# Optimization experiments

Measured on AMD Instinct MI355X. Metric: run time of the kernel, lower is better.

## Reference

```python
import jax, jax.numpy as jnp
import numpy as np

N_NODES = 100000
N_EDGES = 3200000
IN_F, HID, OUT = 3, 32, 1
NEG_SLOPE = 0.2


def _glorot(key, shape):
    fan_in, fan_out = shape[0], shape[-1]
    lim = jnp.sqrt(6.0 / (fan_in + fan_out)).astype(jnp.float32)
    return jax.random.uniform(key, shape, jnp.float32, -lim, lim)


def setup_inputs() -> dict:
    key = jax.random.key(0)
    ks = jax.random.split(key, 12)
    x = jax.random.normal(ks[0], (N_NODES, IN_F), jnp.float32)
    edge_index = jax.random.randint(ks[1], (2, N_EDGES), 0, N_NODES, jnp.int32)
    return {
        "x": x,
        "edge_index": edge_index,
        "W1": _glorot(ks[2], (IN_F, HID)),
        "att_src1": _glorot(ks[3], (1, HID))[0],
        "att_dst1": _glorot(ks[4], (1, HID))[0],
        "b1": jnp.zeros((HID,), jnp.float32),
        "W2": _glorot(ks[5], (HID, HID)),
        "att_src2": _glorot(ks[6], (1, HID))[0],
        "att_dst2": _glorot(ks[7], (1, HID))[0],
        "b2": jnp.zeros((HID,), jnp.float32),
        "Wl": _glorot(ks[8], (HID, OUT)),
        "bl": jnp.zeros((OUT,), jnp.float32),
    }


def gat_layer(x, src, dst, W, att_src, att_dst, b):
    # h: [N, HID] dense transform
    h = x @ W
    # per-node attention halves (compute once per node, gather per edge)
    a_s = h @ att_src  # [N]
    a_d = h @ att_dst  # [N]
    logits = jax.nn.leaky_relu(a_s[src] + a_d[dst], NEG_SLOPE)  # [E+N]
    # segment-softmax over incoming edges of each dst node
    m = jax.ops.segment_max(logits, dst, num_segments=N_NODES)
    m = jnp.where(jnp.isfinite(m), m, 0.0)
    ex = jnp.exp(logits - m[dst])
    denom = jax.ops.segment_sum(ex, dst, num_segments=N_NODES)
    coef = ex / (denom[dst] + 1e-16)
    # weighted scatter-aggregate of source messages
    out = jax.ops.segment_sum(coef[:, None] * h[src], dst, num_segments=N_NODES)
    return out + b


def reference(x, edge_index, W1, att_src1, att_dst1, b1, W2, att_src2, att_dst2, b2, Wl, bl):
    # PyG GATConv default: add self-loops
    loops = jnp.arange(N_NODES, dtype=edge_index.dtype)
    src = jnp.concatenate([edge_index[0], loops])
    dst = jnp.concatenate([edge_index[1], loops])
    h = gat_layer(x, src, dst, W1, att_src1, att_dst1, b1)
    h = jax.nn.relu(h)  # dropout is identity in eval
    h = gat_layer(h, src, dst, W2, att_src2, att_dst2, b2)
    h = jax.nn.relu(h)
    return h @ Wl + bl
```

## Files before the change

kernel.cpp:

```cpp
#include <hip/hip_runtime.h>
#include <hip/hip_fp16.h>

#define HID 32
#define BN 131
#define NBPAD 768
#define BSTRIDE 4608
#define CHUNK 6144
#define EPT 12
#define CPAD 16
#define NSPLIT 3
#define HNMAX 44
#define LPCAP 1700

__device__ __forceinline__ float lrelu(float x) { return x > 0.0f ? x : 0.2f * x; }


__global__ void k_transform1(const float* __restrict__ x,
                             const float* __restrict__ W1,
                             const float* __restrict__ att_src,
                             const float* __restrict__ att_dst,
                             __half* __restrict__ hh,
                             float* __restrict__ a_s,
                             float* __restrict__ a_d,
                             int* __restrict__ cursor, int N)
{
    int tid = blockIdx.x * blockDim.x + threadIdx.x;
    if (tid < NBPAD * CPAD) cursor[tid] = 0;
    int n = tid >> 5, f = tid & 31;
    if (n >= N) return;
    float x0 = x[n * 3 + 0], x1 = x[n * 3 + 1], x2 = x[n * 3 + 2];
    float hv = x0 * W1[f] + x1 * W1[HID + f] + x2 * W1[2 * HID + f];
    hh[(size_t)n * HID + f] = __float2half(hv);
    float as = hv * att_src[f];
    float ad = hv * att_dst[f];
    #pragma unroll
    for (int m = 16; m >= 1; m >>= 1) {
        as += __shfl_xor(as, m, 32);
        ad += __shfl_xor(ad, m, 32);
    }
    if (f == 0) { a_s[n] = as; a_d[n] = ad; }
}


struct BinSM {
    int stage[CHUNK];
    unsigned short sbid[CHUNK];
    int lhist[NBPAD], lexcl[NBPAD], lbase[NBPAD], lcur[NBPAD];
    int arr[256];
};

__global__ void __launch_bounds__(512) k_binscatter(const int* __restrict__ src,
        const int* __restrict__ dst, int* __restrict__ cursor,
        unsigned int* __restrict__ packed, int NBr, int E)
{
    __shared__ BinSM S;
    int t = threadIdx.x;
    int base = blockIdx.x * CHUNK;
    int cnt = E - base; if (cnt > CHUNK) cnt = CHUNK;

    for (int i = t; i < NBPAD; i += 512) { S.lhist[i] = 0; S.lcur[i] = 0; }
    __syncthreads();

    int myd[EPT], mys[EPT];
    #pragma unroll
    for (int u = 0; u < EPT; ++u) {
        int i = t + u * 512;
        myd[u] = -1;
        if (i < cnt) { myd[u] = dst[base + i]; mys[u] = src[base + i]; }
    }
    #pragma unroll
    for (int u = 0; u < EPT; ++u)
        if (myd[u] >= 0) atomicAdd(&S.lhist[myd[u] / BN], 1);
    __syncthreads();

    int b0 = 3 * t;
    int c0 = 0, c1 = 0, c2 = 0, s = 0;
    if (t < 256) {
        c0 = S.lhist[b0]; c1 = S.lhist[b0 + 1]; c2 = S.lhist[b0 + 2];
        s = c0 + c1 + c2;
        S.arr[t] = s;
    }
    __syncthreads();
    for (int o = 1; o < 256; o <<= 1) {
        int v = (t < 256 && t >= o) ? S.arr[t - o] : 0;
        __syncthreads();
        if (t < 256) S.arr[t] += v;
        __syncthreads();
    }
    if (t < 256) {
        int ex = S.arr[t] - s;
        int e0 = ex, e1 = ex + c0, e2 = ex + c0 + c1;
        S.lexcl[b0] = e0; S.lexcl[b0 + 1] = e1; S.lexcl[b0 + 2] = e2;
        for (int i = 0; i < c0; ++i) S.sbid[e0 + i] = (unsigned short)b0;
        for (int i = 0; i < c1; ++i) S.sbid[e1 + i] = (unsigned short)(b0 + 1);
        for (int i = 0; i < c2; ++i) S.sbid[e2 + i] = (unsigned short)(b0 + 2);
    }
    for (int b = t; b < NBr; b += 512)
        if (S.lhist[b])
            S.lbase[b] = b * BSTRIDE + atomicAdd(&cursor[b * CPAD], S.lhist[b]);
    __syncthreads();

    #pragma unroll
    for (int u = 0; u < EPT; ++u) {
        if (myd[u] >= 0) {
            int d = myd[u];
            int b = d / BN;
            int dl = d - b * BN;
            int idx = S.lexcl[b] + atomicAdd(&S.lcur[b], 1);
            S.stage[idx] = (int)((unsigned)mys[u] | ((unsigned)dl << 17));
        }
    }
    __syncthreads();

    for (int i = t; i < cnt; i += 512) {
        int b = S.sbid[i];
        int gpos = S.lbase[b] + (i - S.lexcl[b]);
        if (gpos < (b + 1) * BSTRIDE)
            packed[gpos] = (unsigned)S.stage[i];
    }
}


struct AggSM {
    int2  lpair[LPCAP];
    int   hist[64], scn[64], cur[64];
    float adT[HNMAX];
};

__device__ __forceinline__ void build_slice(AggSM& S,
        const unsigned int* __restrict__ pk, int cnt,
        const float* __restrict__ a_s, const float* __restrict__ a_d,
        int nodeBase, int dlo, int HN, int N)
{
    int t = threadIdx.x;
    if (t < 64) { S.hist[t] = 0; S.cur[t] = 0; }
    if (t < HN) { int n = nodeBase + dlo + t; S.adT[t] = (n < N) ? a_d[n] : 0.0f; }
    __syncthreads();
    for (int i = t; i < cnt; i += 256) {
        unsigned ldl = ((pk[i] >> 17) & 255) - (unsigned)dlo;
        if (ldl < (unsigned)HN) atomicAdd(&S.hist[ldl], 1);
    }
    __syncthreads();
    if (t < 64) S.scn[t] = S.hist[t];
    __syncthreads();
    for (int o = 1; o < 64; o <<= 1) {
        int v = (t < 64 && t >= o) ? S.scn[t - o] : 0;
        __syncthreads();
        if (t < 64) S.scn[t] += v;
        __syncthreads();
    }
    for (int i = t; i < cnt; i += 256) {
        unsigned p = pk[i];
        unsigned ldl = ((p >> 17) & 255) - (unsigned)dlo;
        if (ldl < (unsigned)HN) {
            int sv = (int)(p & 0x1FFFF);
            float e = __expf(lrelu(a_s[sv] + S.adT[ldl]));
            int pos = atomicAdd(&S.cur[ldl], 1);
            int idx = (S.scn[ldl] - S.hist[ldl]) + pos;
            if (idx < LPCAP) S.lpair[idx] = make_int2(sv, __float_as_int(e));
        }
    }
    __syncthreads();
}

__device__ __forceinline__ void agg_node(const __half* __restrict__ hh,
                                         float ex_self, const float* __restrict__ b,
                                         int n, int f,
                                         const int2* lpair,
                                         int off, int dg, float& vx, float& vy)
{
    float den = ex_self;
    float2 hs = __half22float2(*(const __half2*)(hh + (size_t)n * HID + 2 * f));
    float accx = ex_self * hs.x;
    float accy = ex_self * hs.y;
    int j = 0;
    for (; j + 8 <= dg; j += 8) {
        int2 p0 = lpair[off + j + 0], p1 = lpair[off + j + 1];
        int2 p2 = lpair[off + j + 2], p3 = lpair[off + j + 3];
        int2 p4 = lpair[off + j + 4], p5 = lpair[off + j + 5];
        int2 p6 = lpair[off + j + 6], p7 = lpair[off + j + 7];
        __half2 h0 = *(const __half2*)(hh + (size_t)p0.x * HID + 2 * f);
        __half2 h1 = *(const __half2*)(hh + (size_t)p1.x * HID + 2 * f);
        __half2 h2 = *(const __half2*)(hh + (size_t)p2.x * HID + 2 * f);
        __half2 h3 = *(const __half2*)(hh + (size_t)p3.x * HID + 2 * f);
        __half2 h4 = *(const __half2*)(hh + (size_t)p4.x * HID + 2 * f);
        __half2 h5 = *(const __half2*)(hh + (size_t)p5.x * HID + 2 * f);
        __half2 h6 = *(const __half2*)(hh + (size_t)p6.x * HID + 2 * f);
        __half2 h7 = *(const __half2*)(hh + (size_t)p7.x * HID + 2 * f);
        float e0 = __int_as_float(p0.y), e1 = __int_as_float(p1.y);
        float e2 = __int_as_float(p2.y), e3 = __int_as_float(p3.y);
        float e4 = __int_as_float(p4.y), e5 = __int_as_float(p5.y);
        float e6 = __int_as_float(p6.y), e7 = __int_as_float(p7.y);
        float2 q0 = __half22float2(h0), q1 = __half22float2(h1);
        float2 q2 = __half22float2(h2), q3 = __half22float2(h3);
        float2 q4 = __half22float2(h4), q5 = __half22float2(h5);
        float2 q6 = __half22float2(h6), q7 = __half22float2(h7);
        den += ((e0 + e1) + (e2 + e3)) + ((e4 + e5) + (e6 + e7));
        accx = fmaf(e0, q0.x, accx); accy = fmaf(e0, q0.y, accy);
        accx = fmaf(e1, q1.x, accx); accy = fmaf(e1, q1.y, accy);
        accx = fmaf(e2, q2.x, accx); accy = fmaf(e2, q2.y, accy);
        accx = fmaf(e3, q3.x, accx); accy = fmaf(e3, q3.y, accy);
        accx = fmaf(e4, q4.x, accx); accy = fmaf(e4, q4.y, accy);
        accx = fmaf(e5, q5.x, accx); accy = fmaf(e5, q5.y, accy);
        accx = fmaf(e6, q6.x, accx); accy = fmaf(e6, q6.y, accy);
        accx = fmaf(e7, q7.x, accx); accy = fmaf(e7, q7.y, accy);
    }
    for (; j < dg; ++j) {
        int2 p0 = lpair[off + j];
        float e0 = __int_as_float(p0.y);
        float2 q0 = __half22float2(*(const __half2*)(hh + (size_t)p0.x * HID + 2 * f));
        den += e0;
        accx = fmaf(e0, q0.x, accx);
        accy = fmaf(e0, q0.y, accy);
    }
    float inv = 1.0f / (den + 1e-16f);
    vx = fmaxf(accx * inv + b[2 * f], 0.0f);
    vy = fmaxf(accy * inv + b[2 * f + 1], 0.0f);
}

__device__ __forceinline__ void epi_mid(int n, int f, float vx, float vy,
        const float* __restrict__ W2, const float* __restrict__ as2w,
        const float* __restrict__ ad2w,
        __half* __restrict__ hh_out, float* __restrict__ as_out,
        float* __restrict__ ad_out)
{
    float hx = 0.0f, hy = 0.0f;
    #pragma unroll
    for (int k = 0; k < 16; ++k) {
        float va = __shfl(vx, k, 16);
        float vb = __shfl(vy, k, 16);
        float2 w0 = *(const float2*)(W2 + (2 * k) * HID + 2 * f);
        float2 w1 = *(const float2*)(W2 + (2 * k + 1) * HID + 2 * f);
        hx = fmaf(va, w0.x, hx); hy = fmaf(va, w0.y, hy);
        hx = fmaf(vb, w1.x, hx); hy = fmaf(vb, w1.y, hy);
    }
    *(__half2*)(hh_out + (size_t)n * HID + 2 * f) = __floats2half2_rn(hx, hy);
    float as = hx * as2w[2 * f] + hy * as2w[2 * f + 1];
    float ad = hx * ad2w[2 * f] + hy * ad2w[2 * f + 1];
    #pragma unroll
    for (int m2 = 8; m2 >= 1; m2 >>= 1) {
        as += __shfl_xor(as, m2, 16);
        ad += __shfl_xor(ad, m2, 16);
    }
    if (f == 0) { as_out[n] = as; ad_out[n] = ad; }
}


__global__ void __launch_bounds__(256, 8) k_agg_mid(const __half* __restrict__ hh,
        const float* __restrict__ a_s, const float* __restrict__ a_d,
        const int* __restrict__ cursor, const unsigned int* __restrict__ packed,
        const float* __restrict__ b1, const float* __restrict__ W2,
        const float* __restrict__ as2w, const float* __restrict__ ad2w,
        __half* __restrict__ hh_out, float* __restrict__ as_out,
        float* __restrict__ ad_out, int N)
{
    __shared__ AggSM S;
    int bid = blockIdx.x, t = threadIdx.x;
    int bk = bid / NSPLIT, k = bid - NSPLIT * bk;
    int dlo = k * HNMAX;
    int HN = BN - dlo; if (HN > HNMAX) HN = HNMAX;
    int cnt = cursor[bk * CPAD]; if (cnt > BSTRIDE) cnt = BSTRIDE;
    build_slice(S, packed + (size_t)bk * BSTRIDE, cnt, a_s, a_d, bk * BN, dlo, HN, N);
    int g = t >> 4, f = t & 15;
    for (int ldl = g; ldl < HN; ldl += 16) {
        int n = bk * BN + dlo + ldl;
        if (n >= N) continue;
        int off = S.scn[ldl] - S.hist[ldl];
        int dg = S.hist[ldl];
        if (off + dg > LPCAP) dg = LPCAP - off;
        float exs = __expf(lrelu(a_s[n] + S.adT[ldl]));
        float vx, vy;
        agg_node(hh, exs, b1, n, f, S.lpair, off, dg, vx, vy);
        epi_mid(n, f, vx, vy, W2, as2w, ad2w, hh_out, as_out, ad_out);
    }
}

__global__ void __launch_bounds__(256, 8) k_agg_out(const __half* __restrict__ hh,
        const float* __restrict__ a_s, const float* __restrict__ a_d,
        const int* __restrict__ cursor, const unsigned int* __restrict__ packed,
        const float* __restrict__ b2, const float* __restrict__ Wl,
        const float* __restrict__ bl, float* __restrict__ out, int N)
{
    __shared__ AggSM S;
    int bid = blockIdx.x, t = threadIdx.x;
    int bk = bid / NSPLIT, k = bid - NSPLIT * bk;
    int dlo = k * HNMAX;
    int HN = BN - dlo; if (HN > HNMAX) HN = HNMAX;
    int cnt = cursor[bk * CPAD]; if (cnt > BSTRIDE) cnt = BSTRIDE;
    build_slice(S, packed + (size_t)bk * BSTRIDE, cnt, a_s, a_d, bk * BN, dlo, HN, N);
    int g = t >> 4, f = t & 15;
    for (int ldl = g; ldl < HN; ldl += 16) {
        int n = bk * BN + dlo + ldl;
        if (n >= N) continue;
        int off = S.scn[ldl] - S.hist[ldl];
        int dg = S.hist[ldl];
        if (off + dg > LPCAP) dg = LPCAP - off;
        float exs = __expf(lrelu(a_s[n] + S.adT[ldl]));
        float vx, vy;
        agg_node(hh, exs, b2, n, f, S.lpair, off, dg, vx, vy);
        float y = vx * Wl[2 * f] + vy * Wl[2 * f + 1];
        #pragma unroll
        for (int m2 = 8; m2 >= 1; m2 >>= 1)
            y += __shfl_xor(y, m2, 16);
        if (f == 0) out[n] = y + bl[0];
    }
}


extern "C" void kernel_launch(void* const* d_in, const int* in_sizes, int n_in,
                              void* d_out, int out_size, void* d_ws, size_t ws_size,
                              hipStream_t stream)
{
    const float* x        = (const float*)d_in[0];
    const int*   eidx     = (const int*)d_in[1];
    const float* W1       = (const float*)d_in[2];
    const float* att_src1 = (const float*)d_in[3];
    const float* att_dst1 = (const float*)d_in[4];
    const float* b1       = (const float*)d_in[5];
    const float* W2       = (const float*)d_in[6];
    const float* att_src2 = (const float*)d_in[7];
    const float* att_dst2 = (const float*)d_in[8];
    const float* b2       = (const float*)d_in[9];
    const float* Wl       = (const float*)d_in[10];
    const float* bl       = (const float*)d_in[11];
    float* out = (float*)d_out;

    int N = in_sizes[0] / 3;
    int E = in_sizes[1] / 2;
    const int* src = eidx;
    const int* dst = eidx + E;
    int NBr = (N + BN - 1) / BN;

    size_t szNHh = (size_t)N * HID * 2;
    size_t szN4  = (size_t)N * 4;
    size_t szPK  = (size_t)NBr * BSTRIDE * 4;

    char* ws = (char*)d_ws;
    __half* h1h    = (__half*)ws; ws += szNHh;
    __half* h2h    = (__half*)ws; ws += szNHh;
    unsigned int* packed = (unsigned int*)ws; ws += szPK;
    float*  a_s1   = (float*)ws;  ws += szN4;
    float*  a_d1   = (float*)ws;  ws += szN4;
    float*  a_s2   = (float*)ws;  ws += szN4;
    float*  a_d2   = (float*)ws;  ws += szN4;
    int*    cursor = (int*)ws;    ws += (size_t)NBPAD * CPAD * 4;

    const int B = 256;
    int gridNode32 = (N * HID + B - 1) / B;
    int gridBin    = (E + CHUNK - 1) / CHUNK;
    int gridAgg    = NBr * NSPLIT;

    k_transform1<<<gridNode32, B, 0, stream>>>(x, W1, att_src1, att_dst1,
                                               h1h, a_s1, a_d1, cursor, N);
    k_binscatter<<<gridBin, 512, 0, stream>>>(src, dst, cursor, packed, NBr, E);
    k_agg_mid<<<gridAgg, 256, 0, stream>>>(h1h, a_s1, a_d1, cursor, packed,
                                           b1, W2, att_src2, att_dst2,
                                           h2h, a_s2, a_d2, N);
    k_agg_out<<<gridAgg, 256, 0, stream>>>(h2h, a_s2, a_d2, cursor, packed,
                                           b2, Wl, bl, out, N);
}
```

Baseline: 288.3 us.

## Build full-bin CSR once per 512-thread block and software-pipeline neighbor gathers

Aggregation kernels stop splitting each destination bin across three blocks that each rescanned the whole packed bin. Now one 512-thread block builds the complete per-bin CSR in shared memory (36 KB pair buffer) and processes all 131 destinations. This removes the redundant bin scans and exp computations. The inner gather loop is also software-pipelined, loading the next 8 neighbors' features while accumulating the current 8. The trade-offs are larger shared memory, fewer blocks per CU, and more registers.

```diff
diff --git a/kernel.cpp b/kernel.cpp
--- a/kernel.cpp
+++ b/kernel.cpp
@@ -8,9 +8,6 @@
 #define CHUNK 6144
 #define EPT 12
 #define CPAD 16
-#define NSPLIT 3
-#define HNMAX 44
-#define LPCAP 1700
 
 __device__ __forceinline__ float lrelu(float x) { return x > 0.0f ? x : 0.2f * x; }
 
@@ -122,43 +119,38 @@
 
 
 struct AggSM {
-    int2  lpair[LPCAP];
-    int   hist[64], scn[64], cur[64];
-    float adT[HNMAX];
+    int2  lpair[BSTRIDE];
+    int   lhist[256], lscan[256], lcur[256];
+    float adT[BN];
 };
 
-__device__ __forceinline__ void build_slice(AggSM& S,
+__device__ __forceinline__ void build_csr(AggSM& S,
         const unsigned int* __restrict__ pk, int cnt,
         const float* __restrict__ a_s, const float* __restrict__ a_d,
-        int nodeBase, int dlo, int HN, int N)
+        int nodeBase, int N)
 {
     int t = threadIdx.x;
-    if (t < 64) { S.hist[t] = 0; S.cur[t] = 0; }
-    if (t < HN) { int n = nodeBase + dlo + t; S.adT[t] = (n < N) ? a_d[n] : 0.0f; }
-    __syncthreads();
-    for (int i = t; i < cnt; i += 256) {
-        unsigned ldl = ((pk[i] >> 17) & 255) - (unsigned)dlo;
-        if (ldl < (unsigned)HN) atomicAdd(&S.hist[ldl], 1);
-    }
-    __syncthreads();
-    if (t < 64) S.scn[t] = S.hist[t];
-    __syncthreads();
-    for (int o = 1; o < 64; o <<= 1) {
-        int v = (t < 64 && t >= o) ? S.scn[t - o] : 0;
+    if (t < 256) { S.lhist[t] = 0; S.lcur[t] = 0; }
+    if (t < BN) { int n = nodeBase + t; S.adT[t] = (n < N) ? a_d[n] : 0.0f; }
+    __syncthreads();
+    for (int i = t; i < cnt; i += 512)
+        atomicAdd(&S.lhist[(pk[i] >> 17) & 255], 1);
+    __syncthreads();
+    if (t < 256) S.lscan[t] = S.lhist[t];
+    __syncthreads();
+    for (int o = 1; o < 256; o <<= 1) {
+        int v = (t < 256 && t >= o) ? S.lscan[t - o] : 0;
         __syncthreads();
-        if (t < 64) S.scn[t] += v;
+        if (t < 256) S.lscan[t] += v;
         __syncthreads();
     }
-    for (int i = t; i < cnt; i += 256) {
+    for (int i = t; i < cnt; i += 512) {
         unsigned p = pk[i];
-        unsigned ldl = ((p >> 17) & 255) - (unsigned)dlo;
-        if (ldl < (unsigned)HN) {
-            int sv = (int)(p & 0x1FFFF);
-            float e = __expf(lrelu(a_s[sv] + S.adT[ldl]));
-            int pos = atomicAdd(&S.cur[ldl], 1);
-            int idx = (S.scn[ldl] - S.hist[ldl]) + pos;
-            if (idx < LPCAP) S.lpair[idx] = make_int2(sv, __float_as_int(e));
-        }
+        int dl = (p >> 17) & 255;
+        int sv = (int)(p & 0x1FFFF);
+        float e = __expf(lrelu(a_s[sv] + S.adT[dl]));
+        int pos = atomicAdd(&S.lcur[dl], 1);
+        S.lpair[(S.lscan[dl] - S.lhist[dl]) + pos] = make_int2(sv, __float_as_int(e));
     }
     __syncthreads();
 }
@@ -174,44 +166,87 @@
     float accx = ex_self * hs.x;
     float accy = ex_self * hs.y;
     int j = 0;
-    for (; j + 8 <= dg; j += 8) {
-        int2 p0 = lpair[off + j + 0], p1 = lpair[off + j + 1];
-        int2 p2 = lpair[off + j + 2], p3 = lpair[off + j + 3];
-        int2 p4 = lpair[off + j + 4], p5 = lpair[off + j + 5];
-        int2 p6 = lpair[off + j + 6], p7 = lpair[off + j + 7];
-        __half2 h0 = *(const __half2*)(hh + (size_t)p0.x * HID + 2 * f);
-        __half2 h1 = *(const __half2*)(hh + (size_t)p1.x * HID + 2 * f);
-        __half2 h2 = *(const __half2*)(hh + (size_t)p2.x * HID + 2 * f);
-        __half2 h3 = *(const __half2*)(hh + (size_t)p3.x * HID + 2 * f);
-        __half2 h4 = *(const __half2*)(hh + (size_t)p4.x * HID + 2 * f);
-        __half2 h5 = *(const __half2*)(hh + (size_t)p5.x * HID + 2 * f);
-        __half2 h6 = *(const __half2*)(hh + (size_t)p6.x * HID + 2 * f);
-        __half2 h7 = *(const __half2*)(hh + (size_t)p7.x * HID + 2 * f);
-        float e0 = __int_as_float(p0.y), e1 = __int_as_float(p1.y);
-        float e2 = __int_as_float(p2.y), e3 = __int_as_float(p3.y);
-        float e4 = __int_as_float(p4.y), e5 = __int_as_float(p5.y);
-        float e6 = __int_as_float(p6.y), e7 = __int_as_float(p7.y);
-        float2 q0 = __half22float2(h0), q1 = __half22float2(h1);
-        float2 q2 = __half22float2(h2), q3 = __half22float2(h3);
-        float2 q4 = __half22float2(h4), q5 = __half22float2(h5);
-        float2 q6 = __half22float2(h6), q7 = __half22float2(h7);
-        den += ((e0 + e1) + (e2 + e3)) + ((e4 + e5) + (e6 + e7));
-        accx = fmaf(e0, q0.x, accx); accy = fmaf(e0, q0.y, accy);
-        accx = fmaf(e1, q1.x, accx); accy = fmaf(e1, q1.y, accy);
-        accx = fmaf(e2, q2.x, accx); accy = fmaf(e2, q2.y, accy);
-        accx = fmaf(e3, q3.x, accx); accy = fmaf(e3, q3.y, accy);
-        accx = fmaf(e4, q4.x, accx); accy = fmaf(e4, q4.y, accy);
-        accx = fmaf(e5, q5.x, accx); accy = fmaf(e5, q5.y, accy);
-        accx = fmaf(e6, q6.x, accx); accy = fmaf(e6, q6.y, accy);
-        accx = fmaf(e7, q7.x, accx); accy = fmaf(e7, q7.y, accy);
+    if (dg >= 16) {
+        float e0, e1, e2, e3, e4, e5, e6, e7;
+        __half2 g0, g1, g2, g3, g4, g5, g6, g7;
+        {
+            int2 p0 = lpair[off + 0], p1 = lpair[off + 1];
+            int2 p2 = lpair[off + 2], p3 = lpair[off + 3];
+            int2 p4 = lpair[off + 4], p5 = lpair[off + 5];
+            int2 p6 = lpair[off + 6], p7 = lpair[off + 7];
+            g0 = *(const __half2*)(hh + (size_t)p0.x * HID + 2 * f);
+            g1 = *(const __half2*)(hh + (size_t)p1.x * HID + 2 * f);
+            g2 = *(const __half2*)(hh + (size_t)p2.x * HID + 2 * f);
+            g3 = *(const __half2*)(hh + (size_t)p3.x * HID + 2 * f);
+            g4 = *(const __half2*)(hh + (size_t)p4.x * HID + 2 * f);
+            g5 = *(const __half2*)(hh + (size_t)p5.x * HID + 2 * f);
+            g6 = *(const __half2*)(hh + (size_t)p6.x * HID + 2 * f);
+            g7 = *(const __half2*)(hh + (size_t)p7.x * HID + 2 * f);
+            e0 = __int_as_float(p0.y); e1 = __int_as_float(p1.y);
+            e2 = __int_as_float(p2.y); e3 = __int_as_float(p3.y);
+            e4 = __int_as_float(p4.y); e5 = __int_as_float(p5.y);
+            e6 = __int_as_float(p6.y); e7 = __int_as_float(p7.y);
+        }
+        for (; j + 16 <= dg; j += 8) {
+            int jb = off + j + 8;
+            int2 p0 = lpair[jb + 0], p1 = lpair[jb + 1];
+            int2 p2 = lpair[jb + 2], p3 = lpair[jb + 3];
+            int2 p4 = lpair[jb + 4], p5 = lpair[jb + 5];
+            int2 p6 = lpair[jb + 6], p7 = lpair[jb + 7];
+            __half2 t0 = *(const __half2*)(hh + (size_t)p0.x * HID + 2 * f);
+            __half2 t1 = *(const __half2*)(hh + (size_t)p1.x * HID + 2 * f);
+            __half2 t2 = *(const __half2*)(hh + (size_t)p2.x * HID + 2 * f);
+            __half2 t3 = *(const __half2*)(hh + (size_t)p3.x * HID + 2 * f);
+            __half2 t4 = *(const __half2*)(hh + (size_t)p4.x * HID + 2 * f);
+            __half2 t5 = *(const __half2*)(hh + (size_t)p5.x * HID + 2 * f);
+            __half2 t6 = *(const __half2*)(hh + (size_t)p6.x * HID + 2 * f);
+            __half2 t7 = *(const __half2*)(hh + (size_t)p7.x * HID + 2 * f);
+            float u0 = __int_as_float(p0.y), u1 = __int_as_float(p1.y);
+            float u2 = __int_as_float(p2.y), u3 = __int_as_float(p3.y);
+            float u4 = __int_as_float(p4.y), u5 = __int_as_float(p5.y);
+            float u6 = __int_as_float(p6.y), u7 = __int_as_float(p7.y);
+            float2 c0 = __half22float2(g0), c1 = __half22float2(g1);
+            float2 c2 = __half22float2(g2), c3 = __half22float2(g3);
+            float2 c4 = __half22float2(g4), c5 = __half22float2(g5);
+            float2 c6 = __half22float2(g6), c7 = __half22float2(g7);
+            den += ((e0 + e1) + (e2 + e3)) + ((e4 + e5) + (e6 + e7));
+            accx = fmaf(e0, c0.x, accx); accy = fmaf(e0, c0.y, accy);
+            accx = fmaf(e1, c1.x, accx); accy = fmaf(e1, c1.y, accy);
+            accx = fmaf(e2, c2.x, accx); accy = fmaf(e2, c2.y, accy);
+            accx = fmaf(e3, c3.x, accx); accy = fmaf(e3, c3.y, accy);
+            accx = fmaf(e4, c4.x, accx); accy = fmaf(e4, c4.y, accy);
+            accx = fmaf(e5, c5.x, accx); accy = fmaf(e5, c5.y, accy);
+            accx = fmaf(e6, c6.x, accx); accy = fmaf(e6, c6.y, accy);
+            accx = fmaf(e7, c7.x, accx); accy = fmaf(e7, c7.y, accy);
+            e0 = u0; e1 = u1; e2 = u2; e3 = u3;
+            e4 = u4; e5 = u5; e6 = u6; e7 = u7;
+            g0 = t0; g1 = t1; g2 = t2; g3 = t3;
+            g4 = t4; g5 = t5; g6 = t6; g7 = t7;
+        }
+        {
+            float2 c0 = __half22float2(g0), c1 = __half22float2(g1);
+            float2 c2 = __half22float2(g2), c3 = __half22float2(g3);
+            float2 c4 = __half22float2(g4), c5 = __half22float2(g5);
+            float2 c6 = __half22float2(g6), c7 = __half22float2(g7);
+            den += ((e0 + e1) + (e2 + e3)) + ((e4 + e5) + (e6 + e7));
+            accx = fmaf(e0, c0.x, accx); accy = fmaf(e0, c0.y, accy);
+            accx = fmaf(e1, c1.x, accx); accy = fmaf(e1, c1.y, accy);
+            accx = fmaf(e2, c2.x, accx); accy = fmaf(e2, c2.y, accy);
+            accx = fmaf(e3, c3.x, accx); accy = fmaf(e3, c3.y, accy);
+            accx = fmaf(e4, c4.x, accx); accy = fmaf(e4, c4.y, accy);
+            accx = fmaf(e5, c5.x, accx); accy = fmaf(e5, c5.y, accy);
+            accx = fmaf(e6, c6.x, accx); accy = fmaf(e6, c6.y, accy);
+            accx = fmaf(e7, c7.x, accx); accy = fmaf(e7, c7.y, accy);
+        }
+        j += 8;
     }
     for (; j < dg; ++j) {
         int2 p0 = lpair[off + j];
-        float e0 = __int_as_float(p0.y);
-        float2 q0 = __half22float2(*(const __half2*)(hh + (size_t)p0.x * HID + 2 * f));
-        den += e0;
-        accx = fmaf(e0, q0.x, accx);
-        accy = fmaf(e0, q0.y, accy);
+        float ee = __int_as_float(p0.y);
+        float2 cc = __half22float2(*(const __half2*)(hh + (size_t)p0.x * HID + 2 * f));
+        den += ee;
+        accx = fmaf(ee, cc.x, accx);
+        accy = fmaf(ee, cc.y, accy);
     }
     float inv = 1.0f / (den + 1e-16f);
     vx = fmaxf(accx * inv + b[2 * f], 0.0f);
@@ -246,7 +281,7 @@
 }
 
 
-__global__ void __launch_bounds__(256, 8) k_agg_mid(const __half* __restrict__ hh,
+__global__ void __launch_bounds__(512) k_agg_mid(const __half* __restrict__ hh,
         const float* __restrict__ a_s, const float* __restrict__ a_d,
         const int* __restrict__ cursor, const unsigned int* __restrict__ packed,
         const float* __restrict__ b1, const float* __restrict__ W2,
@@ -255,47 +290,39 @@
         float* __restrict__ ad_out, int N)
 {
     __shared__ AggSM S;
-    int bid = blockIdx.x, t = threadIdx.x;
-    int bk = bid / NSPLIT, k = bid - NSPLIT * bk;
-    int dlo = k * HNMAX;
-    int HN = BN - dlo; if (HN > HNMAX) HN = HNMAX;
+    int bk = blockIdx.x, t = threadIdx.x;
     int cnt = cursor[bk * CPAD]; if (cnt > BSTRIDE) cnt = BSTRIDE;
-    build_slice(S, packed + (size_t)bk * BSTRIDE, cnt, a_s, a_d, bk * BN, dlo, HN, N);
+    build_csr(S, packed + (size_t)bk * BSTRIDE, cnt, a_s, a_d, bk * BN, N);
     int g = t >> 4, f = t & 15;
-    for (int ldl = g; ldl < HN; ldl += 16) {
-        int n = bk * BN + dlo + ldl;
+    for (int dl = g; dl < BN; dl += 32) {
+        int n = bk * BN + dl;
         if (n >= N) continue;
-        int off = S.scn[ldl] - S.hist[ldl];
-        int dg = S.hist[ldl];
-        if (off + dg > LPCAP) dg = LPCAP - off;
-        float exs = __expf(lrelu(a_s[n] + S.adT[ldl]));
+        int off = S.lscan[dl] - S.lhist[dl];
+        int dg = S.lhist[dl];
+        float exs = __expf(lrelu(a_s[n] + S.adT[dl]));
         float vx, vy;
         agg_node(hh, exs, b1, n, f, S.lpair, off, dg, vx, vy);
         epi_mid(n, f, vx, vy, W2, as2w, ad2w, hh_out, as_out, ad_out);
     }
 }
 
-__global__ void __launch_bounds__(256, 8) k_agg_out(const __half* __restrict__ hh,
+__global__ void __launch_bounds__(512) k_agg_out(const __half* __restrict__ hh,
         const float* __restrict__ a_s, const float* __restrict__ a_d,
         const int* __restrict__ cursor, const unsigned int* __restrict__ packed,
         const float* __restrict__ b2, const float* __restrict__ Wl,
         const float* __restrict__ bl, float* __restrict__ out, int N)
 {
     __shared__ AggSM S;
-    int bid = blockIdx.x, t = threadIdx.x;
-    int bk = bid / NSPLIT, k = bid - NSPLIT * bk;
-    int dlo = k * HNMAX;
-    int HN = BN - dlo; if (HN > HNMAX) HN = HNMAX;
+    int bk = blockIdx.x, t = threadIdx.x;
     int cnt = cursor[bk * CPAD]; if (cnt > BSTRIDE) cnt = BSTRIDE;
-    build_slice(S, packed + (size_t)bk * BSTRIDE, cnt, a_s, a_d, bk * BN, dlo, HN, N);
+    build_csr(S, packed + (size_t)bk * BSTRIDE, cnt, a_s, a_d, bk * BN, N);
     int g = t >> 4, f = t & 15;
-    for (int ldl = g; ldl < HN; ldl += 16) {
-        int n = bk * BN + dlo + ldl;
+    for (int dl = g; dl < BN; dl += 32) {
+        int n = bk * BN + dl;
         if (n >= N) continue;
-        int off = S.scn[ldl] - S.hist[ldl];
-        int dg = S.hist[ldl];
-        if (off + dg > LPCAP) dg = LPCAP - off;
-        float exs = __expf(lrelu(a_s[n] + S.adT[ldl]));
+        int off = S.lscan[dl] - S.lhist[dl];
+        int dg = S.lhist[dl];
+        float exs = __expf(lrelu(a_s[n] + S.adT[dl]));
         float vx, vy;
         agg_node(hh, exs, b2, n, f, S.lpair, off, dg, vx, vy);
         float y = vx * Wl[2 * f] + vy * Wl[2 * f + 1];
@@ -348,14 +375,13 @@
     const int B = 256;
     int gridNode32 = (N * HID + B - 1) / B;
     int gridBin    = (E + CHUNK - 1) / CHUNK;
-    int gridAgg    = NBr * NSPLIT;
 
     k_transform1<<<gridNode32, B, 0, stream>>>(x, W1, att_src1, att_dst1,
                                                h1h, a_s1, a_d1, cursor, N);
     k_binscatter<<<gridBin, 512, 0, stream>>>(src, dst, cursor, packed, NBr, E);
-    k_agg_mid<<<gridAgg, 256, 0, stream>>>(h1h, a_s1, a_d1, cursor, packed,
-                                           b1, W2, att_src2, att_dst2,
-                                           h2h, a_s2, a_d2, N);
-    k_agg_out<<<gridAgg, 256, 0, stream>>>(h2h, a_s2, a_d2, cursor, packed,
-                                           b2, Wl, bl, out, N);
-}
+    k_agg_mid<<<NBr, 512, 0, stream>>>(h1h, a_s1, a_d1, cursor, packed,
+                                       b1, W2, att_src2, att_dst2,
+                                       h2h, a_s2, a_d2, N);
+    k_agg_out<<<NBr, 512, 0, stream>>>(h2h, a_s2, a_d2, cursor, packed,
+                                       b2, Wl, bl, out, N);
+}
```

Result: faster. 248.6 us (-13.8%).

## Replace 3-way bin slicing with one 512-thread block per smaller bin

Applied to the files above, without the earlier changes.

Each aggregation block used to rescan a whole 131-node bin's packed edges three times, once per 44-node slice. Now bins hold 98 nodes, and one 512-thread block builds the full per-bin CSR once and aggregates all nodes. This removes redundant packed-edge reads and filtering. In exchange it uses more shared memory per block (lpair of 3584 int2), runs a larger scan, and launches fewer, bigger blocks, which may lower occupancy.

```diff
diff --git a/kernel.cpp b/kernel.cpp
--- a/kernel.cpp
+++ b/kernel.cpp
@@ -2,15 +2,12 @@
 #include <hip/hip_fp16.h>
 
 #define HID 32
-#define BN 131
-#define NBPAD 768
-#define BSTRIDE 4608
+#define BN 98
+#define NBPAD 1024
+#define BSTRIDE 3584
 #define CHUNK 6144
 #define EPT 12
 #define CPAD 16
-#define NSPLIT 3
-#define HNMAX 44
-#define LPCAP 1700
 
 __device__ __forceinline__ float lrelu(float x) { return x > 0.0f ? x : 0.2f * x; }
 
@@ -73,11 +70,12 @@
         if (myd[u] >= 0) atomicAdd(&S.lhist[myd[u] / BN], 1);
     __syncthreads();
 
-    int b0 = 3 * t;
-    int c0 = 0, c1 = 0, c2 = 0, s = 0;
+    int b0 = 4 * t;
+    int c0 = 0, c1 = 0, c2 = 0, c3 = 0, s = 0;
     if (t < 256) {
-        c0 = S.lhist[b0]; c1 = S.lhist[b0 + 1]; c2 = S.lhist[b0 + 2];
-        s = c0 + c1 + c2;
+        c0 = S.lhist[b0]; c1 = S.lhist[b0 + 1];
+        c2 = S.lhist[b0 + 2]; c3 = S.lhist[b0 + 3];
+        s = c0 + c1 + c2 + c3;
         S.arr[t] = s;
     }
     __syncthreads();
@@ -89,11 +87,13 @@
     }
     if (t < 256) {
         int ex = S.arr[t] - s;
-        int e0 = ex, e1 = ex + c0, e2 = ex + c0 + c1;
-        S.lexcl[b0] = e0; S.lexcl[b0 + 1] = e1; S.lexcl[b0 + 2] = e2;
+        int e0 = ex, e1 = ex + c0, e2 = e1 + c1, e3 = e2 + c2;
+        S.lexcl[b0] = e0; S.lexcl[b0 + 1] = e1;
+        S.lexcl[b0 + 2] = e2; S.lexcl[b0 + 3] = e3;
         for (int i = 0; i < c0; ++i) S.sbid[e0 + i] = (unsigned short)b0;
         for (int i = 0; i < c1; ++i) S.sbid[e1 + i] = (unsigned short)(b0 + 1);
         for (int i = 0; i < c2; ++i) S.sbid[e2 + i] = (unsigned short)(b0 + 2);
+        for (int i = 0; i < c3; ++i) S.sbid[e3 + i] = (unsigned short)(b0 + 3);
     }
     for (int b = t; b < NBr; b += 512)
         if (S.lhist[b])
@@ -122,43 +122,38 @@
 
 
 struct AggSM {
-    int2  lpair[LPCAP];
-    int   hist[64], scn[64], cur[64];
-    float adT[HNMAX];
+    int2  lpair[BSTRIDE];
+    int   lhist[256], lscan[256], lcur[256];
+    float adT[BN];
 };
 
-__device__ __forceinline__ void build_slice(AggSM& S,
+__device__ __forceinline__ void build_csr(AggSM& S,
         const unsigned int* __restrict__ pk, int cnt,
         const float* __restrict__ a_s, const float* __restrict__ a_d,
-        int nodeBase, int dlo, int HN, int N)
+        int nodeBase, int N)
 {
     int t = threadIdx.x;
-    if (t < 64) { S.hist[t] = 0; S.cur[t] = 0; }
-    if (t < HN) { int n = nodeBase + dlo + t; S.adT[t] = (n < N) ? a_d[n] : 0.0f; }
-    __syncthreads();
-    for (int i = t; i < cnt; i += 256) {
-        unsigned ldl = ((pk[i] >> 17) & 255) - (unsigned)dlo;
-        if (ldl < (unsigned)HN) atomicAdd(&S.hist[ldl], 1);
-    }
-    __syncthreads();
-    if (t < 64) S.scn[t] = S.hist[t];
-    __syncthreads();
-    for (int o = 1; o < 64; o <<= 1) {
-        int v = (t < 64 && t >= o) ? S.scn[t - o] : 0;
+    if (t < 256) { S.lhist[t] = 0; S.lcur[t] = 0; }
+    if (t < BN) { int n = nodeBase + t; S.adT[t] = (n < N) ? a_d[n] : 0.0f; }
+    __syncthreads();
+    for (int i = t; i < cnt; i += 512)
+        atomicAdd(&S.lhist[(pk[i] >> 17) & 255], 1);
+    __syncthreads();
+    if (t < 256) S.lscan[t] = S.lhist[t];
+    __syncthreads();
+    for (int o = 1; o < 256; o <<= 1) {
+        int v = (t < 256 && t >= o) ? S.lscan[t - o] : 0;
         __syncthreads();
-        if (t < 64) S.scn[t] += v;
+        if (t < 256) S.lscan[t] += v;
         __syncthreads();
     }
-    for (int i = t; i < cnt; i += 256) {
+    for (int i = t; i < cnt; i += 512) {
         unsigned p = pk[i];
-        unsigned ldl = ((p >> 17) & 255) - (unsigned)dlo;
-        if (ldl < (unsigned)HN) {
-            int sv = (int)(p & 0x1FFFF);
-            float e = __expf(lrelu(a_s[sv] + S.adT[ldl]));
-            int pos = atomicAdd(&S.cur[ldl], 1);
-            int idx = (S.scn[ldl] - S.hist[ldl]) + pos;
-            if (idx < LPCAP) S.lpair[idx] = make_int2(sv, __float_as_int(e));
-        }
+        int dl = (p >> 17) & 255;
+        int sv = (int)(p & 0x1FFFF);
+        float e = __expf(lrelu(a_s[sv] + S.adT[dl]));
+        int pos = atomicAdd(&S.lcur[dl], 1);
+        S.lpair[(S.lscan[dl] - S.lhist[dl]) + pos] = make_int2(sv, __float_as_int(e));
     }
     __syncthreads();
 }
@@ -246,7 +241,7 @@
 }
 
 
-__global__ void __launch_bounds__(256, 8) k_agg_mid(const __half* __restrict__ hh,
+__global__ void __launch_bounds__(512, 8) k_agg_mid(const __half* __restrict__ hh,
         const float* __restrict__ a_s, const float* __restrict__ a_d,
         const int* __restrict__ cursor, const unsigned int* __restrict__ packed,
         const float* __restrict__ b1, const float* __restrict__ W2,
@@ -255,47 +250,39 @@
         float* __restrict__ ad_out, int N)
 {
     __shared__ AggSM S;
-    int bid = blockIdx.x, t = threadIdx.x;
-    int bk = bid / NSPLIT, k = bid - NSPLIT * bk;
-    int dlo = k * HNMAX;
-    int HN = BN - dlo; if (HN > HNMAX) HN = HNMAX;
+    int bk = blockIdx.x, t = threadIdx.x;
     int cnt = cursor[bk * CPAD]; if (cnt > BSTRIDE) cnt = BSTRIDE;
-    build_slice(S, packed + (size_t)bk * BSTRIDE, cnt, a_s, a_d, bk * BN, dlo, HN, N);
+    build_csr(S, packed + (size_t)bk * BSTRIDE, cnt, a_s, a_d, bk * BN, N);
     int g = t >> 4, f = t & 15;
-    for (int ldl = g; ldl < HN; ldl += 16) {
-        int n = bk * BN + dlo + ldl;
+    for (int dl = g; dl < BN; dl += 32) {
+        int n = bk * BN + dl;
         if (n >= N) continue;
-        int off = S.scn[ldl] - S.hist[ldl];
-        int dg = S.hist[ldl];
-        if (off + dg > LPCAP) dg = LPCAP - off;
-        float exs = __expf(lrelu(a_s[n] + S.adT[ldl]));
+        int off = S.lscan[dl] - S.lhist[dl];
+        int dg = S.lhist[dl];
+        float exs = __expf(lrelu(a_s[n] + S.adT[dl]));
         float vx, vy;
         agg_node(hh, exs, b1, n, f, S.lpair, off, dg, vx, vy);
         epi_mid(n, f, vx, vy, W2, as2w, ad2w, hh_out, as_out, ad_out);
     }
 }
 
-__global__ void __launch_bounds__(256, 8) k_agg_out(const __half* __restrict__ hh,
+__global__ void __launch_bounds__(512, 8) k_agg_out(const __half* __restrict__ hh,
         const float* __restrict__ a_s, const float* __restrict__ a_d,
         const int* __restrict__ cursor, const unsigned int* __restrict__ packed,
         const float* __restrict__ b2, const float* __restrict__ Wl,
         const float* __restrict__ bl, float* __restrict__ out, int N)
 {
     __shared__ AggSM S;
-    int bid = blockIdx.x, t = threadIdx.x;
-    int bk = bid / NSPLIT, k = bid - NSPLIT * bk;
-    int dlo = k * HNMAX;
-    int HN = BN - dlo; if (HN > HNMAX) HN = HNMAX;
+    int bk = blockIdx.x, t = threadIdx.x;
     int cnt = cursor[bk * CPAD]; if (cnt > BSTRIDE) cnt = BSTRIDE;
-    build_slice(S, packed + (size_t)bk * BSTRIDE, cnt, a_s, a_d, bk * BN, dlo, HN, N);
+    build_csr(S, packed + (size_t)bk * BSTRIDE, cnt, a_s, a_d, bk * BN, N);
     int g = t >> 4, f = t & 15;
-    for (int ldl = g; ldl < HN; ldl += 16) {
-        int n = bk * BN + dlo + ldl;
+    for (int dl = g; dl < BN; dl += 32) {
+        int n = bk * BN + dl;
         if (n >= N) continue;
-        int off = S.scn[ldl] - S.hist[ldl];
-        int dg = S.hist[ldl];
-        if (off + dg > LPCAP) dg = LPCAP - off;
-        float exs = __expf(lrelu(a_s[n] + S.adT[ldl]));
+        int off = S.lscan[dl] - S.lhist[dl];
+        int dg = S.lhist[dl];
+        float exs = __expf(lrelu(a_s[n] + S.adT[dl]));
         float vx, vy;
         agg_node(hh, exs, b2, n, f, S.lpair, off, dg, vx, vy);
         float y = vx * Wl[2 * f] + vy * Wl[2 * f + 1];
@@ -348,14 +335,13 @@
     const int B = 256;
     int gridNode32 = (N * HID + B - 1) / B;
     int gridBin    = (E + CHUNK - 1) / CHUNK;
-    int gridAgg    = NBr * NSPLIT;
 
     k_transform1<<<gridNode32, B, 0, stream>>>(x, W1, att_src1, att_dst1,
                                                h1h, a_s1, a_d1, cursor, N);
     k_binscatter<<<gridBin, 512, 0, stream>>>(src, dst, cursor, packed, NBr, E);
-    k_agg_mid<<<gridAgg, 256, 0, stream>>>(h1h, a_s1, a_d1, cursor, packed,
-                                           b1, W2, att_src2, att_dst2,
-                                           h2h, a_s2, a_d2, N);
-    k_agg_out<<<gridAgg, 256, 0, stream>>>(h2h, a_s2, a_d2, cursor, packed,
-                                           b2, Wl, bl, out, N);
-}
+    k_agg_mid<<<NBr, 512, 0, stream>>>(h1h, a_s1, a_d1, cursor, packed,
+                                       b1, W2, att_src2, att_dst2,
+                                       h2h, a_s2, a_d2, N);
+    k_agg_out<<<NBr, 512, 0, stream>>>(h2h, a_s2, a_d2, cursor, packed,
+                                       b2, Wl, bl, out, N);
+}
```

Result: faster. 255.8 us (-11.3%).
